# Performance work log

Measured on AMD Instinct MI355X. Metric: run time of the kernel, lower is better.

The kernel has to match this reference:

```python
import jax, jax.numpy as jnp
import numpy as np

N_NODES = 50000
N_EDGES = 600000
HIDDEN = 128


def _sage_conv(x, src, dst, W_l, W_r, b):
    """PyG SAGEConv with mean aggregation:
    out_i = W_l @ mean_{j in N(i)} x_j + W_r @ x_i + b
    src/dst: [E] edge endpoints (message flows src -> dst).
    """
    msg = x[src]  # [E, d] gather
    agg = jax.ops.segment_sum(msg, dst, num_segments=N_NODES)  # [N, d]
    cnt = jax.ops.segment_sum(jnp.ones((src.shape[0],), x.dtype), dst,
                              num_segments=N_NODES)  # [N]
    mean = agg / jnp.maximum(cnt, 1.0)[:, None]
    return mean @ W_l.T + x @ W_r.T + b


def setup_inputs() -> dict:
    key = jax.random.key(0)
    ks = jax.random.split(key, 12)
    x = jax.random.normal(ks[0], (N_NODES, HIDDEN), dtype=jnp.float32)
    edge_index = jax.random.randint(ks[1], (2, N_EDGES), 0, N_NODES, dtype=jnp.int64)
    scale = 1.0 / np.sqrt(HIDDEN)
    inp = {"x": x, "edge_index": edge_index}
    for i, layer in enumerate(["1", "2", "3"]):
        inp["Wl" + layer] = jax.random.uniform(ks[2 + 3 * i], (HIDDEN, HIDDEN),
                                               minval=-scale, maxval=scale, dtype=jnp.float32)
        inp["Wr" + layer] = jax.random.uniform(ks[3 + 3 * i], (HIDDEN, HIDDEN),
                                               minval=-scale, maxval=scale, dtype=jnp.float32)
        inp["b" + layer] = jax.random.uniform(ks[4 + 3 * i], (HIDDEN,),
                                              minval=-scale, maxval=scale, dtype=jnp.float32)
    return inp


def reference(x, edge_index, Wl1, Wr1, b1, Wl2, Wr2, b2, Wl3, Wr3, b3):
    src, dst = edge_index[0], edge_index[1]
    h = jax.nn.relu(_sage_conv(x, src, dst, Wl1, Wr1, b1))
    h = _sage_conv(h, src, dst, Wl2, Wr2, b2)
    h = _sage_conv(h, src, dst, Wl3, Wr3, b3)
    return h
```

## Files before the change

### kernel.cpp

```cpp
#include <hip/hip_runtime.h>
#include <hip/hip_bf16.h>

#define N_NODES 50000
#define N_EDGES 600000
#define HID 128

typedef __attribute__((ext_vector_type(8))) short s8v;
typedef __attribute__((ext_vector_type(8))) unsigned short u8v;
typedef __attribute__((ext_vector_type(4))) float f4v;

__device__ __forceinline__ unsigned short f2bf(float x) {
    unsigned u = __float_as_uint(x);
    unsigned r = u + 0x7FFFu + ((u >> 16) & 1u);
    return (unsigned short)(r >> 16);
}
__device__ __forceinline__ float bf2f(unsigned short u) {
    return __uint_as_float((unsigned)u << 16);
}
__device__ __forceinline__ void split_bf(float x, unsigned short& hi, unsigned short& lo) {
    hi = f2bf(x);
    lo = f2bf(x - bf2f(hi));
}

__global__ void detect_mode(const void* __restrict__ edges, int* __restrict__ flag) {
    __shared__ int any;
    if (threadIdx.x == 0) any = 0;
    __syncthreads();
    const int* p = (const int*)edges;
    if (p[2 * threadIdx.x + 1] != 0) any = 1;
    __syncthreads();
    if (threadIdx.x == 0) *flag = (any == 0) ? 1 : 0;
}

__device__ __forceinline__ int edge_at(const void* edges, int mode64, long long idx) {
    return mode64 ? (int)((const long long*)edges)[idx] : ((const int*)edges)[idx];
}

__global__ void count_deg(const void* __restrict__ edges, const int* __restrict__ flag,
                          int* __restrict__ deg) {
    int e = blockIdx.x * 256 + threadIdx.x;
    if (e >= N_EDGES) return;
    int m = *flag;
    int d = edge_at(edges, m, (long long)N_EDGES + e);
    if ((unsigned)d < (unsigned)N_NODES) atomicAdd(&deg[d], 1);
}

__global__ void scan_block(const int* __restrict__ deg, int* __restrict__ offs,
                           int* __restrict__ blocksum) {
    __shared__ int sm[256];
    int i = blockIdx.x * 256 + threadIdx.x;
    int v = (i < N_NODES) ? deg[i] : 0;
    sm[threadIdx.x] = v;
    __syncthreads();
    #pragma unroll
    for (int s = 1; s < 256; s <<= 1) {
        int t = (threadIdx.x >= (unsigned)s) ? sm[threadIdx.x - s] : 0;
        __syncthreads();
        sm[threadIdx.x] += t;
        __syncthreads();
    }
    if (i < N_NODES) offs[i] = sm[threadIdx.x] - v;
    if (threadIdx.x == 255) blocksum[blockIdx.x] = sm[255];
}

__global__ void scan_top(int* __restrict__ blocksum, int nblocks) {
    __shared__ int sm[256];
    int v = ((int)threadIdx.x < nblocks) ? blocksum[threadIdx.x] : 0;
    sm[threadIdx.x] = v;
    __syncthreads();
    #pragma unroll
    for (int s = 1; s < 256; s <<= 1) {
        int t = (threadIdx.x >= (unsigned)s) ? sm[threadIdx.x - s] : 0;
        __syncthreads();
        sm[threadIdx.x] += t;
        __syncthreads();
    }
    if ((int)threadIdx.x < nblocks) blocksum[threadIdx.x] = sm[threadIdx.x] - v;
    if (threadIdx.x == 255) blocksum[nblocks] = sm[255];
}

__global__ void scan_add(int* __restrict__ offs, int* __restrict__ cursor,
                         const int* __restrict__ blocksum, int nblocks) {
    int i = blockIdx.x * 256 + threadIdx.x;
    if (i < N_NODES) {
        int o = offs[i] + blocksum[blockIdx.x];
        offs[i] = o;
        cursor[i] = o;
    }
    if (i == 0) offs[N_NODES] = blocksum[nblocks];
}

__global__ void fill_csr(const void* __restrict__ edges, const int* __restrict__ flag,
                         int* __restrict__ cursor, int* __restrict__ csr) {
    int e = blockIdx.x * 256 + threadIdx.x;
    if (e >= N_EDGES) return;
    int m = *flag;
    int d = edge_at(edges, m, (long long)N_EDGES + e);
    int s = edge_at(edges, m, (long long)e);
    if ((unsigned)d >= (unsigned)N_NODES || (unsigned)s >= (unsigned)N_NODES) return;
    int pos = atomicAdd(&cursor[d], 1);
    csr[pos] = s;
}

__global__ void convert_w(const float* __restrict__ m0, const float* __restrict__ m1,
                          const float* __restrict__ m2, const float* __restrict__ m3,
                          const float* __restrict__ m4, const float* __restrict__ m5,
                          unsigned short* __restrict__ whi, unsigned short* __restrict__ wlo) {
    int idx = blockIdx.x * 256 + threadIdx.x;
    if (idx >= 6 * HID * HID) return;
    int mat = idx >> 14, off = idx & 16383;
    const float* src = mat == 0 ? m0 : mat == 1 ? m1 : mat == 2 ? m2
                     : mat == 3 ? m3 : mat == 4 ? m4 : m5;
    unsigned short h, l;
    split_bf(src[off], h, l);
    whi[idx] = h; wlo[idx] = l;
}

__global__ void split_f32(const float* __restrict__ x, unsigned short* __restrict__ hi,
                          unsigned short* __restrict__ lo, int n4) {
    int i = blockIdx.x * 256 + threadIdx.x;
    if (i >= n4) return;
    float4 v = ((const float4*)x)[i];
    ushort4 h, l;
    split_bf(v.x, h.x, l.x);
    split_bf(v.y, h.y, l.y);
    split_bf(v.z, h.z, l.z);
    split_bf(v.w, h.w, l.w);
    ((ushort4*)hi)[i] = h;
    ((ushort4*)lo)[i] = l;
}

__global__ __launch_bounds__(256) void aggregate_bf16(const unsigned short* __restrict__ h,
                                                      const int* __restrict__ offs,
                                                      const int* __restrict__ csr,
                                                      unsigned short* __restrict__ mhi,
                                                      unsigned short* __restrict__ mlo) {
    const int sub  = threadIdx.x & 15;
    const int node = blockIdx.x * 16 + (threadIdx.x >> 4);
    if (node >= N_NODES) return;
    const int beg = offs[node], end = offs[node + 1];
    float a[8] = {0.f, 0.f, 0.f, 0.f, 0.f, 0.f, 0.f, 0.f};
    int p = beg;
    for (; p + 8 <= end; p += 8) {
        int s0 = csr[p],     s1 = csr[p + 1], s2 = csr[p + 2], s3 = csr[p + 3];
        int s4 = csr[p + 4], s5 = csr[p + 5], s6 = csr[p + 6], s7 = csr[p + 7];
        u8v v0 = *(const u8v*)(h + (size_t)s0 * HID + sub * 8);
        u8v v1 = *(const u8v*)(h + (size_t)s1 * HID + sub * 8);
        u8v v2 = *(const u8v*)(h + (size_t)s2 * HID + sub * 8);
        u8v v3 = *(const u8v*)(h + (size_t)s3 * HID + sub * 8);
        u8v v4 = *(const u8v*)(h + (size_t)s4 * HID + sub * 8);
        u8v v5 = *(const u8v*)(h + (size_t)s5 * HID + sub * 8);
        u8v v6 = *(const u8v*)(h + (size_t)s6 * HID + sub * 8);
        u8v v7 = *(const u8v*)(h + (size_t)s7 * HID + sub * 8);
        #pragma unroll
        for (int j = 0; j < 8; ++j)
            a[j] += ((bf2f(v0[j]) + bf2f(v1[j])) + (bf2f(v2[j]) + bf2f(v3[j])))
                  + ((bf2f(v4[j]) + bf2f(v5[j])) + (bf2f(v6[j]) + bf2f(v7[j])));
    }
    if (p + 4 <= end) {
        int s0 = csr[p], s1 = csr[p + 1], s2 = csr[p + 2], s3 = csr[p + 3];
        u8v v0 = *(const u8v*)(h + (size_t)s0 * HID + sub * 8);
        u8v v1 = *(const u8v*)(h + (size_t)s1 * HID + sub * 8);
        u8v v2 = *(const u8v*)(h + (size_t)s2 * HID + sub * 8);
        u8v v3 = *(const u8v*)(h + (size_t)s3 * HID + sub * 8);
        #pragma unroll
        for (int j = 0; j < 8; ++j)
            a[j] += (bf2f(v0[j]) + bf2f(v1[j])) + (bf2f(v2[j]) + bf2f(v3[j]));
        p += 4;
    }
    for (; p < end; ++p) {
        int s = csr[p];
        u8v v = *(const u8v*)(h + (size_t)s * HID + sub * 8);
        #pragma unroll
        for (int j = 0; j < 8; ++j) a[j] += bf2f(v[j]);
    }
    const float inv = 1.0f / fmaxf((float)(end - beg), 1.0f);
    u8v hh, ll;
    #pragma unroll
    for (int j = 0; j < 8; ++j) {
        unsigned short hj, lj;
        split_bf(a[j] * inv, hj, lj);
        hh[j] = hj; ll[j] = lj;
    }
    *(u8v*)(mhi + (size_t)node * HID + sub * 8) = hh;
    *(u8v*)(mlo + (size_t)node * HID + sub * 8) = ll;
}

template <int RELU, int FINAL>
__global__ __launch_bounds__(256) void sage_mfma(
    const unsigned short* __restrict__ Mhi, const unsigned short* __restrict__ Mlo,
    const unsigned short* __restrict__ Hhi, const unsigned short* __restrict__ Hlo,
    const unsigned short* __restrict__ Whi, const unsigned short* __restrict__ Wlo,
    const float* __restrict__ bias,
    unsigned short* __restrict__ ohi, unsigned short* __restrict__ olo,
    float* __restrict__ of32) {
    __shared__ short BhS[128 * 72];
    __shared__ short BlS[128 * 72];
    const int tid = threadIdx.x;
    const int wave = tid >> 6, lane = tid & 63;
    const int mIdx = lane & 15, q = lane >> 4;
    const int wrow = (wave & 1) * 64, wcol = (wave >> 1) * 64;
    const int rowBase = blockIdx.x * 128;

    size_t aoff[4];
    #pragma unroll
    for (int t = 0; t < 4; ++t) {
        int node = rowBase + wrow + t * 16 + mIdx;
        if (node > N_NODES - 1) node = N_NODES - 1;
        aoff[t] = (size_t)node * HID + q * 8;
    }

    const int bcol = tid & 127;
    const int bseg = (tid >> 7) * 32;

    f4v acc[4][4];
    #pragma unroll
    for (int a = 0; a < 4; ++a)
        #pragma unroll
        for (int b = 0; b < 4; ++b) acc[a][b] = (f4v){0.f, 0.f, 0.f, 0.f};

    s8v Ah[2][4], Al[2][4];
    auto loadA = [&](int i, int buf) {
        const unsigned short* ah_ = (i < 4) ? Mhi : Hhi;
        const unsigned short* al_ = (i < 4) ? Mlo : Hlo;
        const int kc = (i & 3) * 32;
        #pragma unroll
        for (int t = 0; t < 4; ++t) {
            Ah[buf][t] = *(const s8v*)(ah_ + aoff[t] + kc);
            Al[buf][t] = *(const s8v*)(al_ + aoff[t] + kc);
        }
    };

    loadA(0, 0);
    for (int panel = 0; panel < 4; ++panel) {
        const int ph = panel >> 1;
        const int kb = (panel & 1) * 64;
        const unsigned short* Wh_ = Whi + ph * HID * HID;
        const unsigned short* Wl_ = Wlo + ph * HID * HID;
        __syncthreads();
        {
            const unsigned short* sh = Wh_ + bcol * HID + kb + bseg;
            const unsigned short* sl = Wl_ + bcol * HID + kb + bseg;
            short* dh = BhS + bcol * 72 + bseg;
            short* dl = BlS + bcol * 72 + bseg;
            #pragma unroll
            for (int j = 0; j < 4; ++j) {
                *(s8v*)(dh + j * 8) = *(const s8v*)(sh + j * 8);
                *(s8v*)(dl + j * 8) = *(const s8v*)(sl + j * 8);
            }
        }
        __syncthreads();
        #pragma unroll
        for (int c = 0; c < 2; ++c) {
            const int i = panel * 2 + c;
            if (i < 7) loadA(i + 1, (i + 1) & 1);
            const int kc2 = c * 32;
            s8v Bh_f[4], Bl_f[4];
            #pragma unroll
            for (int nt = 0; nt < 4; ++nt) {
                const int a = (wcol + nt * 16 + mIdx) * 72 + kc2 + q * 8;
                Bh_f[nt] = *(const s8v*)(BhS + a);
                Bl_f[nt] = *(const s8v*)(BlS + a);
            }
            const int buf = i & 1;
            #pragma unroll
            for (int mt = 0; mt < 4; ++mt)
                #pragma unroll
                for (int nt = 0; nt < 4; ++nt) {
                    acc[mt][nt] = __builtin_amdgcn_mfma_f32_16x16x32_bf16(
                        Ah[buf][mt], Bh_f[nt], acc[mt][nt], 0, 0, 0);
                    acc[mt][nt] = __builtin_amdgcn_mfma_f32_16x16x32_bf16(
                        Al[buf][mt], Bh_f[nt], acc[mt][nt], 0, 0, 0);
                    acc[mt][nt] = __builtin_amdgcn_mfma_f32_16x16x32_bf16(
                        Ah[buf][mt], Bl_f[nt], acc[mt][nt], 0, 0, 0);
                }
        }
    }

    float bv[4];
    #pragma unroll
    for (int nt = 0; nt < 4; ++nt) bv[nt] = bias[wcol + nt * 16 + mIdx];

    #pragma unroll
    for (int mt = 0; mt < 4; ++mt)
        #pragma unroll
        for (int r = 0; r < 4; ++r) {
            int node = rowBase + wrow + mt * 16 + q * 4 + r;
            if (node < N_NODES) {
                #pragma unroll
                for (int nt = 0; nt < 4; ++nt) {
                    int feat = wcol + nt * 16 + mIdx;
                    float v = acc[mt][nt][r] + bv[nt];
                    if (RELU) v = fmaxf(v, 0.f);
                    size_t oidx = (size_t)node * HID + feat;
                    if (FINAL) {
                        of32[oidx] = v;
                    } else {
                        unsigned short hh, ll;
                        split_bf(v, hh, ll);
                        ohi[oidx] = hh;
                        olo[oidx] = ll;
                    }
                }
            }
        }
}

extern "C" void kernel_launch(void* const* d_in, const int* in_sizes, int n_in,
                              void* d_out, int out_size, void* d_ws, size_t ws_size,
                              hipStream_t stream) {
    const float* x   = (const float*)d_in[0];
    const void* edges = d_in[1];
    const float* Wl1 = (const float*)d_in[2];
    const float* Wr1 = (const float*)d_in[3];
    const float* b1  = (const float*)d_in[4];
    const float* Wl2 = (const float*)d_in[5];
    const float* Wr2 = (const float*)d_in[6];
    const float* b2  = (const float*)d_in[7];
    const float* Wl3 = (const float*)d_in[8];
    const float* Wr3 = (const float*)d_in[9];
    const float* b3  = (const float*)d_in[10];
    float* out = (float*)d_out;

    char* ws = (char*)d_ws;
    size_t off = 0;
    auto alloc = [&](size_t bytes) -> void* {
        void* p = (void*)(ws + off);
        off += (bytes + 255) & ~(size_t)255;
        return p;
    };
    typedef unsigned short u16;
    const size_t FEAT = (size_t)N_NODES * HID;
    int* flag     = (int*)alloc(256);
    int* deg      = (int*)alloc((size_t)N_NODES * 4);
    int* offs     = (int*)alloc((size_t)(N_NODES + 1) * 4);
    int* cursor   = (int*)alloc((size_t)N_NODES * 4);
    int* blocksum = (int*)alloc(256 * 4);
    int* csr      = (int*)alloc((size_t)N_EDGES * 4);
    u16* whi      = (u16*)alloc((size_t)6 * HID * HID * 2);
    u16* wlo      = (u16*)alloc((size_t)6 * HID * HID * 2);
    u16* xhi      = (u16*)alloc(FEAT * 2);
    u16* xlo      = (u16*)alloc(FEAT * 2);
    u16* h1hi     = (u16*)alloc(FEAT * 2);
    u16* h1lo     = (u16*)alloc(FEAT * 2);
    u16* mhi      = (u16*)alloc(FEAT * 2);
    u16* mlo      = (u16*)alloc(FEAT * 2);
    (void)ws_size; (void)in_sizes; (void)n_in; (void)out_size;

    const int EB = (N_EDGES + 255) / 256;
    const int NB = (N_NODES + 255) / 256;
    const int AGG_B = (N_NODES + 15) / 16;
    const int GEMM_B = (N_NODES + 127) / 128;
    const int WCV_B = (6 * HID * HID + 255) / 256;
    const int XSP_B = ((int)(FEAT / 4) + 255) / 256;

    hipMemsetAsync(deg, 0, (size_t)N_NODES * 4, stream);
    detect_mode<<<1, 1024, 0, stream>>>(edges, flag);
    count_deg<<<EB, 256, 0, stream>>>(edges, flag, deg);
    scan_block<<<NB, 256, 0, stream>>>(deg, offs, blocksum);
    scan_top<<<1, 256, 0, stream>>>(blocksum, NB);
    scan_add<<<NB, 256, 0, stream>>>(offs, cursor, blocksum, NB);
    fill_csr<<<EB, 256, 0, stream>>>(edges, flag, cursor, csr);

    convert_w<<<WCV_B, 256, 0, stream>>>(Wl1, Wr1, Wl2, Wr2, Wl3, Wr3, whi, wlo);
    split_f32<<<XSP_B, 256, 0, stream>>>(x, xhi, xlo, (int)(FEAT / 4));

    aggregate_bf16<<<AGG_B, 256, 0, stream>>>(xhi, offs, csr, mhi, mlo);
    sage_mfma<1, 0><<<GEMM_B, 256, 0, stream>>>(mhi, mlo, xhi, xlo,
        whi, wlo, b1, h1hi, h1lo, (float*)nullptr);
    aggregate_bf16<<<AGG_B, 256, 0, stream>>>(h1hi, offs, csr, mhi, mlo);
    sage_mfma<0, 0><<<GEMM_B, 256, 0, stream>>>(mhi, mlo, h1hi, h1lo,
        whi + 2 * HID * HID, wlo + 2 * HID * HID, b2, xhi, xlo, (float*)nullptr);
    aggregate_bf16<<<AGG_B, 256, 0, stream>>>(xhi, offs, csr, mhi, mlo);
    sage_mfma<0, 1><<<GEMM_B, 256, 0, stream>>>(mhi, mlo, xhi, xlo,
        whi + 4 * HID * HID, wlo + 4 * HID * HID, b3,
        (u16*)nullptr, (u16*)nullptr, out);
}
```

Measured before the change: 338.0 us.

## Fuse neighbor aggregation into SAGE MFMA GEMM and merge prep kernels

Each SAGE layer now runs as one kernel. It gathers and averages neighbor features for 64 rows directly into shared memory, then runs the split-bf16 MFMA GEMM on them, so the mean-message buffers are no longer written to and read back from global memory. The degree count, weight conversion and x splitting are merged into one multi-role prep kernel, and edge-format detection becomes a per-wave ballot, which removes several launches and the flag buffer. In exchange the GEMM tile shrinks from 128 to 64 rows and the aggregation is no longer overlapped with the GEMM. Occupancy now depends on the larger shared-memory footprint and the launch_bounds setting.

```diff
diff --git a/kernel.cpp b/kernel.cpp
--- a/kernel.cpp
+++ b/kernel.cpp
@@ -22,27 +22,56 @@
     lo = f2bf(x - bf2f(hi));
 }
 
-__global__ void detect_mode(const void* __restrict__ edges, int* __restrict__ flag) {
-    __shared__ int any;
-    if (threadIdx.x == 0) any = 0;
-    __syncthreads();
+__device__ __forceinline__ int detect_m64(const void* edges) {
     const int* p = (const int*)edges;
-    if (p[2 * threadIdx.x + 1] != 0) any = 1;
-    __syncthreads();
-    if (threadIdx.x == 0) *flag = (any == 0) ? 1 : 0;
+    int lane = threadIdx.x & 63;
+    unsigned long long nz = __ballot(p[2 * lane + 1] != 0);
+    return (nz == 0ULL) ? 1 : 0;
 }
 
 __device__ __forceinline__ int edge_at(const void* edges, int mode64, long long idx) {
     return mode64 ? (int)((const long long*)edges)[idx] : ((const int*)edges)[idx];
 }
 
-__global__ void count_deg(const void* __restrict__ edges, const int* __restrict__ flag,
-                          int* __restrict__ deg) {
-    int e = blockIdx.x * 256 + threadIdx.x;
-    if (e >= N_EDGES) return;
-    int m = *flag;
-    int d = edge_at(edges, m, (long long)N_EDGES + e);
-    if ((unsigned)d < (unsigned)N_NODES) atomicAdd(&deg[d], 1);
+__global__ __launch_bounds__(256) void prep(
+    const void* __restrict__ edges, const float* __restrict__ x,
+    const float* __restrict__ m0, const float* __restrict__ m1,
+    const float* __restrict__ m2, const float* __restrict__ m3,
+    const float* __restrict__ m4, const float* __restrict__ m5,
+    int* __restrict__ deg,
+    unsigned short* __restrict__ whi, unsigned short* __restrict__ wlo,
+    unsigned short* __restrict__ xhi, unsigned short* __restrict__ xlo) {
+    const int EB  = (N_EDGES + 255) / 256;
+    const int WCV = (6 * HID * HID + 255) / 256;
+    const int b = blockIdx.x;
+    if (b < EB) {
+        int m = detect_m64(edges);
+        int e = b * 256 + threadIdx.x;
+        if (e >= N_EDGES) return;
+        int d = edge_at(edges, m, (long long)N_EDGES + e);
+        if ((unsigned)d < (unsigned)N_NODES) atomicAdd(&deg[d], 1);
+    } else if (b < EB + WCV) {
+        int idx = (b - EB) * 256 + threadIdx.x;
+        if (idx >= 6 * HID * HID) return;
+        int mat = idx >> 14, off = idx & 16383;
+        const float* src = mat == 0 ? m0 : mat == 1 ? m1 : mat == 2 ? m2
+                         : mat == 3 ? m3 : mat == 4 ? m4 : m5;
+        unsigned short h, l;
+        split_bf(src[off], h, l);
+        whi[idx] = h; wlo[idx] = l;
+    } else {
+        const int n4 = (N_NODES * HID) / 4;
+        int i = (b - EB - WCV) * 256 + threadIdx.x;
+        if (i >= n4) return;
+        float4 v = ((const float4*)x)[i];
+        ushort4 h, l;
+        split_bf(v.x, h.x, l.x);
+        split_bf(v.y, h.y, l.y);
+        split_bf(v.z, h.z, l.z);
+        split_bf(v.w, h.w, l.w);
+        ((ushort4*)xhi)[i] = h;
+        ((ushort4*)xlo)[i] = l;
+    }
 }
 
 __global__ void scan_block(const int* __restrict__ deg, int* __restrict__ offs,
@@ -90,11 +119,11 @@
     if (i == 0) offs[N_NODES] = blocksum[nblocks];
 }
 
-__global__ void fill_csr(const void* __restrict__ edges, const int* __restrict__ flag,
+__global__ void fill_csr(const void* __restrict__ edges,
                          int* __restrict__ cursor, int* __restrict__ csr) {
+    int m = detect_m64(edges);
     int e = blockIdx.x * 256 + threadIdx.x;
     if (e >= N_EDGES) return;
-    int m = *flag;
     int d = edge_at(edges, m, (long long)N_EDGES + e);
     int s = edge_at(edges, m, (long long)e);
     if ((unsigned)d >= (unsigned)N_NODES || (unsigned)s >= (unsigned)N_NODES) return;
@@ -102,136 +131,103 @@
     csr[pos] = s;
 }
 
-__global__ void convert_w(const float* __restrict__ m0, const float* __restrict__ m1,
-                          const float* __restrict__ m2, const float* __restrict__ m3,
-                          const float* __restrict__ m4, const float* __restrict__ m5,
-                          unsigned short* __restrict__ whi, unsigned short* __restrict__ wlo) {
-    int idx = blockIdx.x * 256 + threadIdx.x;
-    if (idx >= 6 * HID * HID) return;
-    int mat = idx >> 14, off = idx & 16383;
-    const float* src = mat == 0 ? m0 : mat == 1 ? m1 : mat == 2 ? m2
-                     : mat == 3 ? m3 : mat == 4 ? m4 : m5;
-    unsigned short h, l;
-    split_bf(src[off], h, l);
-    whi[idx] = h; wlo[idx] = l;
-}
-
-__global__ void split_f32(const float* __restrict__ x, unsigned short* __restrict__ hi,
-                          unsigned short* __restrict__ lo, int n4) {
-    int i = blockIdx.x * 256 + threadIdx.x;
-    if (i >= n4) return;
-    float4 v = ((const float4*)x)[i];
-    ushort4 h, l;
-    split_bf(v.x, h.x, l.x);
-    split_bf(v.y, h.y, l.y);
-    split_bf(v.z, h.z, l.z);
-    split_bf(v.w, h.w, l.w);
-    ((ushort4*)hi)[i] = h;
-    ((ushort4*)lo)[i] = l;
-}
-
-__global__ __launch_bounds__(256) void aggregate_bf16(const unsigned short* __restrict__ h,
-                                                      const int* __restrict__ offs,
-                                                      const int* __restrict__ csr,
-                                                      unsigned short* __restrict__ mhi,
-                                                      unsigned short* __restrict__ mlo) {
-    const int sub  = threadIdx.x & 15;
-    const int node = blockIdx.x * 16 + (threadIdx.x >> 4);
-    if (node >= N_NODES) return;
-    const int beg = offs[node], end = offs[node + 1];
-    float a[8] = {0.f, 0.f, 0.f, 0.f, 0.f, 0.f, 0.f, 0.f};
-    int p = beg;
-    for (; p + 8 <= end; p += 8) {
-        int s0 = csr[p],     s1 = csr[p + 1], s2 = csr[p + 2], s3 = csr[p + 3];
-        int s4 = csr[p + 4], s5 = csr[p + 5], s6 = csr[p + 6], s7 = csr[p + 7];
-        u8v v0 = *(const u8v*)(h + (size_t)s0 * HID + sub * 8);
-        u8v v1 = *(const u8v*)(h + (size_t)s1 * HID + sub * 8);
-        u8v v2 = *(const u8v*)(h + (size_t)s2 * HID + sub * 8);
-        u8v v3 = *(const u8v*)(h + (size_t)s3 * HID + sub * 8);
-        u8v v4 = *(const u8v*)(h + (size_t)s4 * HID + sub * 8);
-        u8v v5 = *(const u8v*)(h + (size_t)s5 * HID + sub * 8);
-        u8v v6 = *(const u8v*)(h + (size_t)s6 * HID + sub * 8);
-        u8v v7 = *(const u8v*)(h + (size_t)s7 * HID + sub * 8);
-        #pragma unroll
-        for (int j = 0; j < 8; ++j)
-            a[j] += ((bf2f(v0[j]) + bf2f(v1[j])) + (bf2f(v2[j]) + bf2f(v3[j])))
-                  + ((bf2f(v4[j]) + bf2f(v5[j])) + (bf2f(v6[j]) + bf2f(v7[j])));
-    }
-    if (p + 4 <= end) {
-        int s0 = csr[p], s1 = csr[p + 1], s2 = csr[p + 2], s3 = csr[p + 3];
-        u8v v0 = *(const u8v*)(h + (size_t)s0 * HID + sub * 8);
-        u8v v1 = *(const u8v*)(h + (size_t)s1 * HID + sub * 8);
-        u8v v2 = *(const u8v*)(h + (size_t)s2 * HID + sub * 8);
-        u8v v3 = *(const u8v*)(h + (size_t)s3 * HID + sub * 8);
-        #pragma unroll
-        for (int j = 0; j < 8; ++j)
-            a[j] += (bf2f(v0[j]) + bf2f(v1[j])) + (bf2f(v2[j]) + bf2f(v3[j]));
-        p += 4;
-    }
-    for (; p < end; ++p) {
-        int s = csr[p];
-        u8v v = *(const u8v*)(h + (size_t)s * HID + sub * 8);
-        #pragma unroll
-        for (int j = 0; j < 8; ++j) a[j] += bf2f(v[j]);
-    }
-    const float inv = 1.0f / fmaxf((float)(end - beg), 1.0f);
-    u8v hh, ll;
-    #pragma unroll
-    for (int j = 0; j < 8; ++j) {
-        unsigned short hj, lj;
-        split_bf(a[j] * inv, hj, lj);
-        hh[j] = hj; ll[j] = lj;
-    }
-    *(u8v*)(mhi + (size_t)node * HID + sub * 8) = hh;
-    *(u8v*)(mlo + (size_t)node * HID + sub * 8) = ll;
-}
-
 template <int RELU, int FINAL>
-__global__ __launch_bounds__(256) void sage_mfma(
-    const unsigned short* __restrict__ Mhi, const unsigned short* __restrict__ Mlo,
+__global__ __launch_bounds__(256, 2) void sage_fused(
     const unsigned short* __restrict__ Hhi, const unsigned short* __restrict__ Hlo,
+    const int* __restrict__ offs, const int* __restrict__ csr,
     const unsigned short* __restrict__ Whi, const unsigned short* __restrict__ Wlo,
     const float* __restrict__ bias,
     unsigned short* __restrict__ ohi, unsigned short* __restrict__ olo,
     float* __restrict__ of32) {
+    __shared__ short Mh[64 * 136];
+    __shared__ short Ml[64 * 136];
     __shared__ short BhS[128 * 72];
     __shared__ short BlS[128 * 72];
+
     const int tid = threadIdx.x;
     const int wave = tid >> 6, lane = tid & 63;
     const int mIdx = lane & 15, q = lane >> 4;
-    const int wrow = (wave & 1) * 64, wcol = (wave >> 1) * 64;
-    const int rowBase = blockIdx.x * 128;
-
-    size_t aoff[4];
-    #pragma unroll
-    for (int t = 0; t < 4; ++t) {
-        int node = rowBase + wrow + t * 16 + mIdx;
+    const int wrow = (wave & 1) * 32, wcol = (wave >> 1) * 64;
+    const int rowBase = blockIdx.x * 64;
+
+    size_t aoff[2];
+    #pragma unroll
+    for (int mt = 0; mt < 2; ++mt) {
+        int node = rowBase + wrow + mt * 16 + mIdx;
         if (node > N_NODES - 1) node = N_NODES - 1;
-        aoff[t] = (size_t)node * HID + q * 8;
-    }
-
-    const int bcol = tid & 127;
-    const int bseg = (tid >> 7) * 32;
-
-    f4v acc[4][4];
-    #pragma unroll
-    for (int a = 0; a < 4; ++a)
+        aoff[mt] = (size_t)node * HID + q * 8;
+    }
+    s8v Hh[2][4], Hl[2][4];
+    #pragma unroll
+    for (int mt = 0; mt < 2; ++mt)
+        #pragma unroll
+        for (int c = 0; c < 4; ++c) {
+            Hh[mt][c] = *(const s8v*)(Hhi + aoff[mt] + c * 32);
+            Hl[mt][c] = *(const s8v*)(Hlo + aoff[mt] + c * 32);
+        }
+
+    const int sub = tid & 15;
+    const int grp = tid >> 4;
+    for (int it = 0; it < 4; ++it) {
+        const int r = it * 16 + grp;
+        const int node = rowBase + r;
+        float a[8] = {0.f, 0.f, 0.f, 0.f, 0.f, 0.f, 0.f, 0.f};
+        float inv = 1.0f;
+        if (node < N_NODES) {
+            const int beg = offs[node], end = offs[node + 1];
+            int p = beg;
+            for (; p + 8 <= end; p += 8) {
+                int s0 = csr[p],     s1 = csr[p + 1], s2 = csr[p + 2], s3 = csr[p + 3];
+                int s4 = csr[p + 4], s5 = csr[p + 5], s6 = csr[p + 6], s7 = csr[p + 7];
+                u8v v0 = *(const u8v*)(Hhi + (size_t)s0 * HID + sub * 8);
+                u8v v1 = *(const u8v*)(Hhi + (size_t)s1 * HID + sub * 8);
+                u8v v2 = *(const u8v*)(Hhi + (size_t)s2 * HID + sub * 8);
+                u8v v3 = *(const u8v*)(Hhi + (size_t)s3 * HID + sub * 8);
+                u8v v4 = *(const u8v*)(Hhi + (size_t)s4 * HID + sub * 8);
+                u8v v5 = *(const u8v*)(Hhi + (size_t)s5 * HID + sub * 8);
+                u8v v6 = *(const u8v*)(Hhi + (size_t)s6 * HID + sub * 8);
+                u8v v7 = *(const u8v*)(Hhi + (size_t)s7 * HID + sub * 8);
+                #pragma unroll
+                for (int j = 0; j < 8; ++j)
+                    a[j] += ((bf2f(v0[j]) + bf2f(v1[j])) + (bf2f(v2[j]) + bf2f(v3[j])))
+                          + ((bf2f(v4[j]) + bf2f(v5[j])) + (bf2f(v6[j]) + bf2f(v7[j])));
+            }
+            if (p + 4 <= end) {
+                int s0 = csr[p], s1 = csr[p + 1], s2 = csr[p + 2], s3 = csr[p + 3];
+                u8v v0 = *(const u8v*)(Hhi + (size_t)s0 * HID + sub * 8);
+                u8v v1 = *(const u8v*)(Hhi + (size_t)s1 * HID + sub * 8);
+                u8v v2 = *(const u8v*)(Hhi + (size_t)s2 * HID + sub * 8);
+                u8v v3 = *(const u8v*)(Hhi + (size_t)s3 * HID + sub * 8);
+                #pragma unroll
+                for (int j = 0; j < 8; ++j)
+                    a[j] += (bf2f(v0[j]) + bf2f(v1[j])) + (bf2f(v2[j]) + bf2f(v3[j]));
+                p += 4;
+            }
+            for (; p < end; ++p) {
+                int s = csr[p];
+                u8v v = *(const u8v*)(Hhi + (size_t)s * HID + sub * 8);
+                #pragma unroll
+                for (int j = 0; j < 8; ++j) a[j] += bf2f(v[j]);
+            }
+            inv = 1.0f / fmaxf((float)(end - beg), 1.0f);
+        }
+        u8v hh, ll;
+        #pragma unroll
+        for (int j = 0; j < 8; ++j) {
+            unsigned short hj, lj;
+            split_bf(a[j] * inv, hj, lj);
+            hh[j] = hj; ll[j] = lj;
+        }
+        *(u8v*)(Mh + r * 136 + sub * 8) = hh;
+        *(u8v*)(Ml + r * 136 + sub * 8) = ll;
+    }
+
+    f4v acc[2][4];
+    #pragma unroll
+    for (int a = 0; a < 2; ++a)
         #pragma unroll
         for (int b = 0; b < 4; ++b) acc[a][b] = (f4v){0.f, 0.f, 0.f, 0.f};
 
-    s8v Ah[2][4], Al[2][4];
-    auto loadA = [&](int i, int buf) {
-        const unsigned short* ah_ = (i < 4) ? Mhi : Hhi;
-        const unsigned short* al_ = (i < 4) ? Mlo : Hlo;
-        const int kc = (i & 3) * 32;
-        #pragma unroll
-        for (int t = 0; t < 4; ++t) {
-            Ah[buf][t] = *(const s8v*)(ah_ + aoff[t] + kc);
-            Al[buf][t] = *(const s8v*)(al_ + aoff[t] + kc);
-        }
-    };
-
-    loadA(0, 0);
     for (int panel = 0; panel < 4; ++panel) {
         const int ph = panel >> 1;
         const int kb = (panel & 1) * 64;
@@ -239,6 +235,8 @@
         const unsigned short* Wl_ = Wlo + ph * HID * HID;
         __syncthreads();
         {
+            const int bcol = tid & 127;
+            const int bseg = (tid >> 7) * 32;
             const unsigned short* sh = Wh_ + bcol * HID + kb + bseg;
             const unsigned short* sl = Wl_ + bcol * HID + kb + bseg;
             short* dh = BhS + bcol * 72 + bseg;
@@ -252,8 +250,6 @@
         __syncthreads();
         #pragma unroll
         for (int c = 0; c < 2; ++c) {
-            const int i = panel * 2 + c;
-            if (i < 7) loadA(i + 1, (i + 1) & 1);
             const int kc2 = c * 32;
             s8v Bh_f[4], Bl_f[4];
             #pragma unroll
@@ -262,17 +258,32 @@
                 Bh_f[nt] = *(const s8v*)(BhS + a);
                 Bl_f[nt] = *(const s8v*)(BlS + a);
             }
-            const int buf = i & 1;
+            s8v Ah_f[2], Al_f[2];
+            if (panel < 2) {
+                #pragma unroll
+                for (int mt = 0; mt < 2; ++mt) {
+                    const int a = (wrow + mt * 16 + mIdx) * 136 + kb + kc2 + q * 8;
+                    Ah_f[mt] = *(const s8v*)(Mh + a);
+                    Al_f[mt] = *(const s8v*)(Ml + a);
+                }
+            } else {
+                const int idx = (panel - 2) * 2 + c;
+                #pragma unroll
+                for (int mt = 0; mt < 2; ++mt) {
+                    Ah_f[mt] = Hh[mt][idx];
+                    Al_f[mt] = Hl[mt][idx];
+                }
+            }
             #pragma unroll
-            for (int mt = 0; mt < 4; ++mt)
+            for (int mt = 0; mt < 2; ++mt)
                 #pragma unroll
                 for (int nt = 0; nt < 4; ++nt) {
                     acc[mt][nt] = __builtin_amdgcn_mfma_f32_16x16x32_bf16(
-                        Ah[buf][mt], Bh_f[nt], acc[mt][nt], 0, 0, 0);
+                        Ah_f[mt], Bh_f[nt], acc[mt][nt], 0, 0, 0);
                     acc[mt][nt] = __builtin_amdgcn_mfma_f32_16x16x32_bf16(
-                        Al[buf][mt], Bh_f[nt], acc[mt][nt], 0, 0, 0);
+                        Al_f[mt], Bh_f[nt], acc[mt][nt], 0, 0, 0);
                     acc[mt][nt] = __builtin_amdgcn_mfma_f32_16x16x32_bf16(
-                        Ah[buf][mt], Bl_f[nt], acc[mt][nt], 0, 0, 0);
+                        Ah_f[mt], Bl_f[nt], acc[mt][nt], 0, 0, 0);
                 }
         }
     }
@@ -282,7 +293,7 @@
     for (int nt = 0; nt < 4; ++nt) bv[nt] = bias[wcol + nt * 16 + mIdx];
 
     #pragma unroll
-    for (int mt = 0; mt < 4; ++mt)
+    for (int mt = 0; mt < 2; ++mt)
         #pragma unroll
         for (int r = 0; r < 4; ++r) {
             int node = rowBase + wrow + mt * 16 + q * 4 + r;
@@ -331,7 +342,6 @@
     };
     typedef unsigned short u16;
     const size_t FEAT = (size_t)N_NODES * HID;
-    int* flag     = (int*)alloc(256);
     int* deg      = (int*)alloc((size_t)N_NODES * 4);
     int* offs     = (int*)alloc((size_t)(N_NODES + 1) * 4);
     int* cursor   = (int*)alloc((size_t)N_NODES * 4);
@@ -343,36 +353,28 @@
     u16* xlo      = (u16*)alloc(FEAT * 2);
     u16* h1hi     = (u16*)alloc(FEAT * 2);
     u16* h1lo     = (u16*)alloc(FEAT * 2);
-    u16* mhi      = (u16*)alloc(FEAT * 2);
-    u16* mlo      = (u16*)alloc(FEAT * 2);
     (void)ws_size; (void)in_sizes; (void)n_in; (void)out_size;
 
-    const int EB = (N_EDGES + 255) / 256;
-    const int NB = (N_NODES + 255) / 256;
-    const int AGG_B = (N_NODES + 15) / 16;
-    const int GEMM_B = (N_NODES + 127) / 128;
-    const int WCV_B = (6 * HID * HID + 255) / 256;
-    const int XSP_B = ((int)(FEAT / 4) + 255) / 256;
+    const int EB    = (N_EDGES + 255) / 256;
+    const int NB    = (N_NODES + 255) / 256;
+    const int WCV   = (6 * HID * HID + 255) / 256;
+    const int XSP   = ((int)(FEAT / 4) + 255) / 256;
+    const int PREPB = EB + WCV + XSP;
+    const int FUSE_B = (N_NODES + 63) / 64;
 
     hipMemsetAsync(deg, 0, (size_t)N_NODES * 4, stream);
-    detect_mode<<<1, 1024, 0, stream>>>(edges, flag);
-    count_deg<<<EB, 256, 0, stream>>>(edges, flag, deg);
+    prep<<<PREPB, 256, 0, stream>>>(edges, x, Wl1, Wr1, Wl2, Wr2, Wl3, Wr3,
+                                    deg, whi, wlo, xhi, xlo);
     scan_block<<<NB, 256, 0, stream>>>(deg, offs, blocksum);
     scan_top<<<1, 256, 0, stream>>>(blocksum, NB);
     scan_add<<<NB, 256, 0, stream>>>(offs, cursor, blocksum, NB);
-    fill_csr<<<EB, 256, 0, stream>>>(edges, flag, cursor, csr);
-
-    convert_w<<<WCV_B, 256, 0, stream>>>(Wl1, Wr1, Wl2, Wr2, Wl3, Wr3, whi, wlo);
-    split_f32<<<XSP_B, 256, 0, stream>>>(x, xhi, xlo, (int)(FEAT / 4));
-
-    aggregate_bf16<<<AGG_B, 256, 0, stream>>>(xhi, offs, csr, mhi, mlo);
-    sage_mfma<1, 0><<<GEMM_B, 256, 0, stream>>>(mhi, mlo, xhi, xlo,
+    fill_csr<<<EB, 256, 0, stream>>>(edges, cursor, csr);
+
+    sage_fused<1, 0><<<FUSE_B, 256, 0, stream>>>(xhi, xlo, offs, csr,
         whi, wlo, b1, h1hi, h1lo, (float*)nullptr);
-    aggregate_bf16<<<AGG_B, 256, 0, stream>>>(h1hi, offs, csr, mhi, mlo);
-    sage_mfma<0, 0><<<GEMM_B, 256, 0, stream>>>(mhi, mlo, h1hi, h1lo,
+    sage_fused<0, 0><<<FUSE_B, 256, 0, stream>>>(h1hi, h1lo, offs, csr,
         whi + 2 * HID * HID, wlo + 2 * HID * HID, b2, xhi, xlo, (float*)nullptr);
-    aggregate_bf16<<<AGG_B, 256, 0, stream>>>(xhi, offs, csr, mhi, mlo);
-    sage_mfma<0, 1><<<GEMM_B, 256, 0, stream>>>(mhi, mlo, xhi, xlo,
+    sage_fused<0, 1><<<FUSE_B, 256, 0, stream>>>(xhi, xlo, offs, csr,
         whi + 4 * HID * HID, wlo + 4 * HID * HID, b3,
         (u16*)nullptr, (u16*)nullptr, out);
 }
```

New measurement: 369.2 us. 1.09x slower.
